# Performance work log

Measured on AMD Instinct MI355X. Metric: run time of the kernel, lower is better.

The kernel has to match this reference:

```python
import jax, jax.numpy as jnp
from jax import lax
import numpy as np

B, T, V, E, H = 2048, 512, 4, 64, 128


def setup_inputs() -> dict:
    key = jax.random.key(0)
    ks = jax.random.split(key, 8)
    s = 0.1  # small init scale
    x = jax.random.randint(ks[0], (B, T), 0, V, dtype=jnp.int64)
    emb = jax.random.normal(ks[1], (V, E), dtype=jnp.float32) * s
    W_ih = jax.random.normal(ks[2], (3 * H, E), dtype=jnp.float32) * s
    W_hh = jax.random.normal(ks[3], (3 * H, H), dtype=jnp.float32) * s
    b_ih = jax.random.normal(ks[4], (3 * H,), dtype=jnp.float32) * s
    b_hh = jax.random.normal(ks[5], (3 * H,), dtype=jnp.float32) * s
    W_fc = jax.random.normal(ks[6], (V, H), dtype=jnp.float32) * s
    b_fc = jax.random.normal(ks[7], (V,), dtype=jnp.float32) * s
    return {"x": x, "emb": emb, "W_ih": W_ih, "W_hh": W_hh,
            "b_ih": b_ih, "b_hh": b_hh, "W_fc": W_fc, "b_fc": b_fc}


def reference(x, emb, W_ih, W_hh, b_ih, b_hh, W_fc, b_fc):
    # Embedding lookup: [B, T, E]
    xe = emb[x]
    # Precompute all input-side gate projections in one big GEMM: [B, T, 3H]
    gi = jnp.einsum("bte,ge->btg", xe, W_ih) + b_ih
    gi = jnp.swapaxes(gi, 0, 1)  # [T, B, 3H] for scan over time

    def step(h, gi_t):
        # PyTorch GRU gate order: r, z, n
        gi_r, gi_z, gi_n = jnp.split(gi_t, 3, axis=-1)
        gh = h @ W_hh.T + b_hh  # [B, 3H]
        gh_r, gh_z, gh_n = jnp.split(gh, 3, axis=-1)
        r = jax.nn.sigmoid(gi_r + gh_r)
        z = jax.nn.sigmoid(gi_z + gh_z)
        n = jnp.tanh(gi_n + r * gh_n)
        h_new = (1.0 - z) * n + z * h
        return h_new, None

    h0 = jnp.zeros((x.shape[0], H), dtype=gi.dtype)
    hT, _ = lax.scan(step, h0, gi)  # only final hidden state is needed
    logits = hT @ W_fc.T + b_fc  # [B, V]
    return logits
```

## Files before the change

kernel.cpp:

```cpp
#include <hip/hip_runtime.h>
#include <hip/hip_bf16.h>


#define B_  2048
#define T_  512
#define V_  4
#define E_  64
#define H_  128
#define G3  384
#define G3P 392
#define SH  136

#define LOG2E 1.4426950408889634f

typedef __attribute__((ext_vector_type(8))) short  short8;
typedef __attribute__((ext_vector_type(4))) float  float4v;
typedef __attribute__((ext_vector_type(2))) float  f32x2;
typedef unsigned long long ull;

__device__ __forceinline__ short bf16s(float f) {
  union { float ff; unsigned int u; } c; c.ff = f;
  return (short)((c.u + 0x7fffu + ((c.u >> 16) & 1u)) >> 16);
}

__global__ void gi_table_kernel(const float* __restrict__ emb,
                                const float* __restrict__ W_ih,
                                const float* __restrict__ b_ih,
                                const float* __restrict__ b_hh,
                                float* __restrict__ table) {
  int gid = blockIdx.x * blockDim.x + threadIdx.x;
  if (gid >= V_ * G3) return;
  int v = gid / G3;
  int g = gid - v * G3;
  float acc = b_ih[g];
  if (g < 2 * H_) acc += b_hh[g];
  const float* wr = W_ih + g * E_;
  const float* er = emb + v * E_;
#pragma unroll 8
  for (int e = 0; e < E_; ++e) acc += wr[e] * er[e];
  table[gid] = acc * ((g < 2 * H_) ? -LOG2E : 2.f * LOG2E);
}

#define MFMA16(A, B, C) __builtin_amdgcn_mfma_f32_16x16x32_bf16((A), (B), (C), 0, 0, 0)

__global__ __launch_bounds__(512) void gru_kernel(
    const int* __restrict__ x, const float* __restrict__ W_hh,
    const float* __restrict__ b_hh, const float* __restrict__ W_fc,
    const float* __restrict__ b_fc, const float* __restrict__ table,
    float* __restrict__ out) {
  __shared__ __align__(16) short hbuf[2][16 * SH];
  __shared__ __align__(16) unsigned char xs[(T_ + 2) * 16];
  __shared__ __align__(16) float tabS[V_ * G3P];
  __shared__ __align__(16) float hf[16 * H_];

  const int tid  = threadIdx.x;
  const int w    = tid >> 6;
  const int lane = tid & 63;
  const int m    = lane & 15;
  const int q    = lane >> 4;
  const int g0   = blockIdx.x * 16;

  for (int i = tid; i < 16 * T_; i += 512) {
    int r = i >> 9;
    int t = i & (T_ - 1);
    xs[t * 16 + r] = (unsigned char)(x[(g0 + r) * T_ + t] & 3);
  }
  if (tid < 32) xs[T_ * 16 + tid] = 0;
  for (int v = 0; v < V_; ++v)
    for (int g = tid; g < G3; g += 512) tabS[v * G3P + g] = table[v * G3 + g];
  for (int i = tid; i < 16 * SH; i += 512) hbuf[0][i] = 0;

  short8 wA[3][4];
#pragma unroll
  for (int s = 0; s < 3; ++s) {
    const float sc = (s < 2) ? -LOG2E : 2.f * LOG2E;
    const float* wrow = W_hh + (s * H_ + w * 16 + m) * H_;
#pragma unroll
    for (int ks = 0; ks < 4; ++ks) {
      const float* p = wrow + ks * 32 + q * 8;
      short8 f;
#pragma unroll
      for (int jj = 0; jj < 8; ++jj) f[jj] = bf16s(p[jj] * sc);
      wA[s][ks] = f;
    }
  }

  const int c0 = w * 16 + q * 4;
  float4v bhnC;
  {
    const float* p = b_hh + 2 * H_ + c0;
#pragma unroll
    for (int i = 0; i < 4; ++i) bhnC[i] = p[i] * 2.f * LOG2E;
  }
  f32x2 hA = {0.f, 0.f}, hB = {0.f, 0.f};

  __syncthreads();

  float4v gAR, gAZ, gAN, gBR, gBZ, gBN;
  int vb;
  {
    int v0 = xs[m] & 3;
    const float* tb = &tabS[v0 * G3P + c0];
    gAR = *(const float4v*)(tb);
    gAZ = *(const float4v*)(tb + H_);
    gAN = *(const float4v*)(tb + 2 * H_);
    vb  = xs[16 + m];
  }

  const f32x2 one2 = {1.f, 1.f};

  auto step = [&](int FROM, int TO, int t,
                  float4v& guR, float4v& guZ, float4v& guN,
                  float4v& glR, float4v& glZ, float4v& glN) {
    const short* rbp = &hbuf[FROM][m * SH + q * 8];
    short8 h0 = *(const short8*)(rbp);
    short8 h1 = *(const short8*)(rbp + 32);
    short8 h2 = *(const short8*)(rbp + 64);
    short8 h3 = *(const short8*)(rbp + 96);

    float4v a0 = MFMA16(wA[0][0], h0, guR);
    a0 = MFMA16(wA[0][1], h1, a0);
    a0 = MFMA16(wA[0][2], h2, a0);
    a0 = MFMA16(wA[0][3], h3, a0);
    float4v a2 = MFMA16(wA[2][0], h0, bhnC);
    a2 = MFMA16(wA[2][1], h1, a2);
    a2 = MFMA16(wA[2][2], h2, a2);
    a2 = MFMA16(wA[2][3], h3, a2);
    float4v a1 = MFMA16(wA[1][0], h0, guZ);
    a1 = MFMA16(wA[1][1], h1, a1);
    a1 = MFMA16(wA[1][2], h2, a1);
    a1 = MFMA16(wA[1][3], h3, a1);

    float r0 = __builtin_amdgcn_rcpf(1.f + __builtin_amdgcn_exp2f(a0[0]));
    float r1 = __builtin_amdgcn_rcpf(1.f + __builtin_amdgcn_exp2f(a0[1]));
    float r2 = __builtin_amdgcn_rcpf(1.f + __builtin_amdgcn_exp2f(a0[2]));
    float r3 = __builtin_amdgcn_rcpf(1.f + __builtin_amdgcn_exp2f(a0[3]));

    int vb2 = xs[(t + 2) * 16 + m];
    const float* tbn = &tabS[(vb & 3) * G3P + c0];
    glR = *(const float4v*)(tbn);
    glZ = *(const float4v*)(tbn + H_);
    glN = *(const float4v*)(tbn + 2 * H_);
    vb = vb2;

    f32x2 rA = {r0, r1},           rB = {r2, r3};
    f32x2 a2A = {a2[0], a2[1]},    a2B = {a2[2], a2[3]};
    f32x2 gnA = {guN[0], guN[1]},  gnB = {guN[2], guN[3]};
    f32x2 npA = rA * a2A + gnA;
    f32x2 npB = rB * a2B + gnB;
    f32x2 eA = {__builtin_amdgcn_exp2f(npA.x), __builtin_amdgcn_exp2f(npA.y)};
    f32x2 eB = {__builtin_amdgcn_exp2f(npB.x), __builtin_amdgcn_exp2f(npB.y)};
    f32x2 EzA = {__builtin_amdgcn_exp2f(a1[0]), __builtin_amdgcn_exp2f(a1[1])};
    f32x2 EzB = {__builtin_amdgcn_exp2f(a1[2]), __builtin_amdgcn_exp2f(a1[3])};
    f32x2 numA = eA * (EzA + hA) + (hA - EzA);
    f32x2 numB = eB * (EzB + hB) + (hB - EzB);
    f32x2 denA = (eA + one2) * (one2 + EzA);
    f32x2 denB = (eB + one2) * (one2 + EzB);
    f32x2 rcA = {__builtin_amdgcn_rcpf(denA.x), __builtin_amdgcn_rcpf(denA.y)};
    f32x2 rcB = {__builtin_amdgcn_rcpf(denB.x), __builtin_amdgcn_rcpf(denB.y)};
    hA = numA * rcA;
    hB = numB * rcB;
    unsigned int pk0, pk1;
    asm("v_cvt_pk_bf16_f32 %0, %1, %2" : "=v"(pk0) : "v"(hA.x), "v"(hA.y));
    asm("v_cvt_pk_bf16_f32 %0, %1, %2" : "=v"(pk1) : "v"(hB.x), "v"(hB.y));
    *(ull*)(&hbuf[TO][m * SH + c0]) = ((ull)pk1 << 32) | pk0;
    __syncthreads();
  };

  for (int t = 0; t < T_; t += 2) {
    step(0, 1, t,     gAR, gAZ, gAN, gBR, gBZ, gBN);
    step(1, 0, t + 1, gBR, gBZ, gBN, gAR, gAZ, gAN);
  }

  hf[m * H_ + c0 + 0] = hA.x;
  hf[m * H_ + c0 + 1] = hA.y;
  hf[m * H_ + c0 + 2] = hB.x;
  hf[m * H_ + c0 + 3] = hB.y;
  __syncthreads();

  if (tid < 64) {
    int row = tid >> 2, vo = tid & 3;
    float s = b_fc[vo];
    const float* wv = W_fc + vo * H_;
    const float* hr = &hf[row * H_];
#pragma unroll 4
    for (int k = 0; k < H_; k += 4)
      s += hr[k] * wv[k] + hr[k + 1] * wv[k + 1]
         + hr[k + 2] * wv[k + 2] + hr[k + 3] * wv[k + 3];
    out[(g0 + row) * V_ + vo] = s;
  }
}

extern "C" void kernel_launch(void* const* d_in, const int* in_sizes, int n_in,
                              void* d_out, int out_size, void* d_ws, size_t ws_size,
                              hipStream_t stream) {
  const int*   x    = (const int*)d_in[0];
  const float* emb  = (const float*)d_in[1];
  const float* W_ih = (const float*)d_in[2];
  const float* W_hh = (const float*)d_in[3];
  const float* b_ih = (const float*)d_in[4];
  const float* b_hh = (const float*)d_in[5];
  const float* W_fc = (const float*)d_in[6];
  const float* b_fc = (const float*)d_in[7];
  float* out   = (float*)d_out;
  float* table = (float*)d_ws;

  gi_table_kernel<<<(V_ * G3 + 255) / 256, 256, 0, stream>>>(emb, W_ih, b_ih, b_hh, table);
  gru_kernel<<<B_ / 16, 512, 0, stream>>>(x, W_hh, b_hh, W_fc, b_fc, table, out);
}
```

Before: 315.4 us.

## Halve batch rows per block to fill all CUs, duplicating rows in MFMA

Each block now processes 8 batch rows instead of 16, doubling the grid so every compute unit gets a block. The 16-row MFMA tile is filled by writing each hidden row twice, and lanes split the 4 accumulator columns so each computes only 2 gate outputs. This trades wasted MFMA throughput (half the tile is duplicated) for more parallelism and less per-lane elementwise work on the serial recurrence.

```diff
diff --git a/kernel.cpp b/kernel.cpp
--- a/kernel.cpp
+++ b/kernel.cpp
@@ -10,13 +10,13 @@
 #define G3  384
 #define G3P 392
 #define SH  136
+#define NB  8
 
 #define LOG2E 1.4426950408889634f
 
 typedef __attribute__((ext_vector_type(8))) short  short8;
 typedef __attribute__((ext_vector_type(4))) float  float4v;
 typedef __attribute__((ext_vector_type(2))) float  f32x2;
-typedef unsigned long long ull;
 
 __device__ __forceinline__ short bf16s(float f) {
   union { float ff; unsigned int u; } c; c.ff = f;
@@ -49,26 +49,28 @@
     const float* __restrict__ b_fc, const float* __restrict__ table,
     float* __restrict__ out) {
   __shared__ __align__(16) short hbuf[2][16 * SH];
-  __shared__ __align__(16) unsigned char xs[(T_ + 2) * 16];
+  __shared__ __align__(16) unsigned char xs[(T_ + 2) * NB];
   __shared__ __align__(16) float tabS[V_ * G3P];
-  __shared__ __align__(16) float hf[16 * H_];
+  __shared__ __align__(16) float hf[NB * H_];
 
   const int tid  = threadIdx.x;
   const int w    = tid >> 6;
   const int lane = tid & 63;
   const int m    = lane & 15;
   const int q    = lane >> 4;
-  const int g0   = blockIdx.x * 16;
-
-  for (int i = tid; i < 16 * T_; i += 512) {
+  const int mb   = m & 7;
+  const bool isHi = (m & 8) != 0;
+  const int g0   = blockIdx.x * NB;
+
+  for (int i = tid; i < NB * T_; i += 512) {
     int r = i >> 9;
     int t = i & (T_ - 1);
-    xs[t * 16 + r] = (unsigned char)(x[(g0 + r) * T_ + t] & 3);
-  }
-  if (tid < 32) xs[T_ * 16 + tid] = 0;
+    xs[t * NB + r] = (unsigned char)(x[(g0 + r) * T_ + t] & 3);
+  }
+  if (tid < 16) xs[T_ * NB + tid] = 0;
   for (int v = 0; v < V_; ++v)
     for (int g = tid; g < G3; g += 512) tabS[v * G3P + g] = table[v * G3 + g];
-  for (int i = tid; i < 16 * SH; i += 512) hbuf[0][i] = 0;
+  for (int i = tid; i < 2 * 16 * SH; i += 512) hbuf[0][i] = 0;
 
   short8 wA[3][4];
 #pragma unroll
@@ -85,33 +87,42 @@
     }
   }
 
-  const int c0 = w * 16 + q * 4;
+  const int c0  = w * 16 + q * 4;
+  const int c0r = c0 + (isHi ? 2 : 0);
   float4v bhnC;
   {
     const float* p = b_hh + 2 * H_ + c0;
 #pragma unroll
     for (int i = 0; i < 4; ++i) bhnC[i] = p[i] * 2.f * LOG2E;
   }
-  f32x2 hA = {0.f, 0.f}, hB = {0.f, 0.f};
+  f32x2 hA = {0.f, 0.f};
 
   __syncthreads();
 
-  float4v gAR, gAZ, gAN, gBR, gBZ, gBN;
+  float4v gAR, gAZ, gBR, gBZ;
+  f32x2 gAN, gBN;
   int vb;
   {
-    int v0 = xs[m] & 3;
+    int v0 = xs[mb] & 3;
     const float* tb = &tabS[v0 * G3P + c0];
     gAR = *(const float4v*)(tb);
     gAZ = *(const float4v*)(tb + H_);
-    gAN = *(const float4v*)(tb + 2 * H_);
-    vb  = xs[16 + m];
+    gAN = *(const f32x2*)(&tabS[v0 * G3P + 2 * H_ + c0r]);
+    vb  = xs[NB + mb];
   }
 
   const f32x2 one2 = {1.f, 1.f};
 
+  auto sel = [&](const float4v& xv) -> f32x2 {
+    f32x2 r;
+    r.x = isHi ? xv[2] : xv[0];
+    r.y = isHi ? xv[3] : xv[1];
+    return r;
+  };
+
   auto step = [&](int FROM, int TO, int t,
-                  float4v& guR, float4v& guZ, float4v& guN,
-                  float4v& glR, float4v& glZ, float4v& glN) {
+                  float4v& guR, float4v& guZ, f32x2& guN,
+                  float4v& glR, float4v& glZ, f32x2& glN) {
     const short* rbp = &hbuf[FROM][m * SH + q * 8];
     short8 h0 = *(const short8*)(rbp);
     short8 h1 = *(const short8*)(rbp + 32);
@@ -131,39 +142,31 @@
     a1 = MFMA16(wA[1][2], h2, a1);
     a1 = MFMA16(wA[1][3], h3, a1);
 
-    float r0 = __builtin_amdgcn_rcpf(1.f + __builtin_amdgcn_exp2f(a0[0]));
-    float r1 = __builtin_amdgcn_rcpf(1.f + __builtin_amdgcn_exp2f(a0[1]));
-    float r2 = __builtin_amdgcn_rcpf(1.f + __builtin_amdgcn_exp2f(a0[2]));
-    float r3 = __builtin_amdgcn_rcpf(1.f + __builtin_amdgcn_exp2f(a0[3]));
-
-    int vb2 = xs[(t + 2) * 16 + m];
+    f32x2 a0e = sel(a0);
+    f32x2 rr;
+    rr.x = __builtin_amdgcn_rcpf(1.f + __builtin_amdgcn_exp2f(a0e.x));
+    rr.y = __builtin_amdgcn_rcpf(1.f + __builtin_amdgcn_exp2f(a0e.y));
+    f32x2 a2e = sel(a2);
+    f32x2 a1e = sel(a1);
+
+    int vb2 = xs[(t + 2) * NB + mb];
     const float* tbn = &tabS[(vb & 3) * G3P + c0];
     glR = *(const float4v*)(tbn);
     glZ = *(const float4v*)(tbn + H_);
-    glN = *(const float4v*)(tbn + 2 * H_);
+    glN = *(const f32x2*)(tbn + 2 * H_ + (isHi ? 2 : 0));
     vb = vb2;
 
-    f32x2 rA = {r0, r1},           rB = {r2, r3};
-    f32x2 a2A = {a2[0], a2[1]},    a2B = {a2[2], a2[3]};
-    f32x2 gnA = {guN[0], guN[1]},  gnB = {guN[2], guN[3]};
-    f32x2 npA = rA * a2A + gnA;
-    f32x2 npB = rB * a2B + gnB;
-    f32x2 eA = {__builtin_amdgcn_exp2f(npA.x), __builtin_amdgcn_exp2f(npA.y)};
-    f32x2 eB = {__builtin_amdgcn_exp2f(npB.x), __builtin_amdgcn_exp2f(npB.y)};
-    f32x2 EzA = {__builtin_amdgcn_exp2f(a1[0]), __builtin_amdgcn_exp2f(a1[1])};
-    f32x2 EzB = {__builtin_amdgcn_exp2f(a1[2]), __builtin_amdgcn_exp2f(a1[3])};
-    f32x2 numA = eA * (EzA + hA) + (hA - EzA);
-    f32x2 numB = eB * (EzB + hB) + (hB - EzB);
-    f32x2 denA = (eA + one2) * (one2 + EzA);
-    f32x2 denB = (eB + one2) * (one2 + EzB);
-    f32x2 rcA = {__builtin_amdgcn_rcpf(denA.x), __builtin_amdgcn_rcpf(denA.y)};
-    f32x2 rcB = {__builtin_amdgcn_rcpf(denB.x), __builtin_amdgcn_rcpf(denB.y)};
-    hA = numA * rcA;
-    hB = numB * rcB;
-    unsigned int pk0, pk1;
+    f32x2 np = rr * a2e + guN;
+    f32x2 e  = {__builtin_amdgcn_exp2f(np.x), __builtin_amdgcn_exp2f(np.y)};
+    f32x2 Ez = {__builtin_amdgcn_exp2f(a1e.x), __builtin_amdgcn_exp2f(a1e.y)};
+    f32x2 num = e * (Ez + hA) + (hA - Ez);
+    f32x2 den = (e + one2) * (one2 + Ez);
+    f32x2 rc  = {__builtin_amdgcn_rcpf(den.x), __builtin_amdgcn_rcpf(den.y)};
+    hA = num * rc;
+    unsigned int pk0;
     asm("v_cvt_pk_bf16_f32 %0, %1, %2" : "=v"(pk0) : "v"(hA.x), "v"(hA.y));
-    asm("v_cvt_pk_bf16_f32 %0, %1, %2" : "=v"(pk1) : "v"(hB.x), "v"(hB.y));
-    *(ull*)(&hbuf[TO][m * SH + c0]) = ((ull)pk1 << 32) | pk0;
+    *(unsigned int*)(&hbuf[TO][mb * SH + c0r]) = pk0;
+    *(unsigned int*)(&hbuf[TO][(mb + 8) * SH + c0r]) = pk0;
     __syncthreads();
   };
 
@@ -172,13 +175,11 @@
     step(1, 0, t + 1, gBR, gBZ, gBN, gAR, gAZ, gAN);
   }
 
-  hf[m * H_ + c0 + 0] = hA.x;
-  hf[m * H_ + c0 + 1] = hA.y;
-  hf[m * H_ + c0 + 2] = hB.x;
-  hf[m * H_ + c0 + 3] = hB.y;
+  hf[mb * H_ + c0r + 0] = hA.x;
+  hf[mb * H_ + c0r + 1] = hA.y;
   __syncthreads();
 
-  if (tid < 64) {
+  if (tid < 32) {
     int row = tid >> 2, vo = tid & 3;
     float s = b_fc[vo];
     const float* wv = W_fc + vo * H_;
@@ -206,5 +207,5 @@
   float* table = (float*)d_ws;
 
   gi_table_kernel<<<(V_ * G3 + 255) / 256, 256, 0, stream>>>(emb, W_ih, b_ih, b_hh, table);
-  gru_kernel<<<B_ / 16, 512, 0, stream>>>(x, W_hh, b_hh, W_fc, b_fc, table, out);
-}
+  gru_kernel<<<B_ / NB, 512, 0, stream>>>(x, W_hh, b_hh, W_fc, b_fc, table, out);
+}
```

Result: faster. 285.3 us (-9.5%).
